# Kernel optimization log

Measured on AMD Instinct MI355X. Metric: run time of the kernel, lower is better.

## Reference

```python
import jax, jax.numpy as jnp
import numpy as np

B, S, H, K = 64, 512, 768, 64
NR, NN, ND = 9, 3, 3


def setup_inputs() -> dict:
    key = jax.random.key(0)
    ks = jax.random.split(key, 20)
    inp = {}
    inp["sequence_output"] = jax.random.normal(ks[0], (B, S, H), jnp.float32)
    for i, name in enumerate(["rel", "nov", "dir"]):
        inp[f"{name}_idx"] = jax.random.randint(ks[1 + i], (B, K), 0, S)
        inp[f"{name}_len"] = jax.random.randint(ks[4 + i], (B,), 0, K + 1)
    scale = 0.02
    for i, (name, nlab) in enumerate([("rel", NR), ("nov", NN), ("dir", ND)]):
        k0, k1 = jax.random.split(ks[7 + i])
        inp[f"{name}_dense_W"] = scale * jax.random.normal(k0, (H, H), jnp.float32)
        inp[f"{name}_dense_b"] = jnp.zeros((H,), jnp.float32)
        inp[f"{name}_cls_W"] = scale * jax.random.normal(k1, (nlab, H), jnp.float32)
        inp[f"{name}_cls_b"] = jnp.zeros((nlab,), jnp.float32)
    return inp


def _attn_pool(seq, idx, length):
    """Ragged intra-group self-attention pooling (get_token_reps / get_ne_reps).

    seq: [B,S,H]; idx: [B,K] padded token indices; length: [B] valid counts.
    Original computes (softmax(G G^T) @ G)[0]; only row 0 of the attention is
    needed, so we compute just that row.
    """
    G = jnp.take_along_axis(seq, idx[:, :, None], axis=1)  # [B,K,H]
    mask = jnp.arange(idx.shape[1])[None, :] < length[:, None]  # [B,K]
    scores0 = jnp.einsum('bh,bjh->bj', G[:, 0], G)  # row 0 of G G^T
    scores0 = jnp.where(mask, scores0, jnp.float32(-1e30))
    a0 = jax.nn.softmax(scores0, axis=-1)  # [B,K]
    pooled = jnp.einsum('bj,bjh->bh', a0, G)  # [B,H]
    # empty-group fallback: sequence_output[b, 0]
    return jnp.where(length[:, None] > 0, pooled, seq[:, 0])


def _head(rep, Wd, bd, Wc, bc):
    # HiddenTokenPooler dense + tanh, then token classifier
    h = jnp.tanh(rep @ Wd.T + bd)
    return h @ Wc.T + bc


def reference(sequence_output, rel_idx, rel_len, nov_idx, nov_len, dir_idx, dir_len,
              rel_dense_W, rel_dense_b, rel_cls_W, rel_cls_b,
              nov_dense_W, nov_dense_b, nov_cls_W, nov_cls_b,
              dir_dense_W, dir_dense_b, dir_cls_W, dir_cls_b):
    rel_rep = _attn_pool(sequence_output, rel_idx, rel_len)
    nov_rep = _attn_pool(sequence_output, nov_idx, nov_len)
    dir_rep = _attn_pool(sequence_output, dir_idx, dir_len)
    rel_logits = _head(rel_rep, rel_dense_W, rel_dense_b, rel_cls_W, rel_cls_b)
    nov_logits = _head(nov_rep, nov_dense_W, nov_dense_b, nov_cls_W, nov_cls_b)
    dir_logits = _head(dir_rep, dir_dense_W, dir_dense_b, dir_cls_W, dir_cls_b)
    return (rel_logits, nov_logits, dir_logits)
```

## Files before the change

kernel.cpp:

```cpp
#include <hip/hip_runtime.h>
#include <math.h>


#define Hdim 768
#define Kdim 64
#define Sdim 512
#define Bdim 64

typedef float f32x4 __attribute__((ext_vector_type(4)));
typedef short bf16x8 __attribute__((ext_vector_type(8)));

__device__ __forceinline__ unsigned short f2bf(float f) {
    union { float f; unsigned int u; } c; c.f = f;
    unsigned int u = c.u + 0x7FFFu + ((c.u >> 16) & 1u);
    return (unsigned short)(u >> 16);
}

__device__ __forceinline__ void cvt8(const float* __restrict__ src,
                                     unsigned short* __restrict__ dst) {
    float4 x = *(const float4*)src, y = *(const float4*)(src + 4);
    *(ushort4*)dst       = make_ushort4(f2bf(x.x), f2bf(x.y), f2bf(x.z), f2bf(x.w));
    *(ushort4*)(dst + 4) = make_ushort4(f2bf(y.x), f2bf(y.y), f2bf(y.z), f2bf(y.w));
}

__global__ __launch_bounds__(1024) void k_pool(
    const float* __restrict__ seq,
    const int* __restrict__ idxr, const int* __restrict__ lenr,
    const int* __restrict__ idxn, const int* __restrict__ lenn,
    const int* __restrict__ idxd, const int* __restrict__ lend,
    const float* __restrict__ cbr, const float* __restrict__ cbn,
    const float* __restrict__ cbd,
    const float* __restrict__ dWr, const float* __restrict__ dWn,
    const float* __restrict__ dWd,
    unsigned short* __restrict__ Wbf,
    unsigned short* __restrict__ Pbf,
    float* __restrict__ out)
{
    const int b = blockIdx.x, g = blockIdx.y;
    const int tid = threadIdx.x, lane = tid & 63, wave = tid >> 6;

    const int* idxp = (g == 0) ? idxr : (g == 1) ? idxn : idxd;
    const int* lnp  = (g == 0) ? lenr : (g == 1) ? lenn : lend;

    __shared__ int   sidx[Kdim];
    __shared__ float wm[16], wl[16], coef[16];
    __shared__ float wpart[16][Hdim];

    if (tid < Kdim) sidx[tid] = idxp[b * Kdim + tid];
    const int len = lnp[b];

    if (b == 0) {
        if (g == 0)      { if (tid < 576) out[tid]       = cbr[tid % 9]; }
        else if (g == 1) { if (tid < 192) out[576 + tid] = cbn[tid % 3]; }
        else             { if (tid < 192) out[768 + tid] = cbd[tid % 3]; }
    }
    __syncthreads();

    unsigned short* Pb = Pbf + ((size_t)g * Bdim + b) * Hdim;

    if (len > 0) {
        const float* row0 = seq + ((size_t)b * Sdim + sidx[0]) * Hdim;
        float g0[12];
#pragma unroll
        for (int k = 0; k < 3; ++k) {
            float4 v = *(const float4*)(row0 + 4 * lane + 256 * k);
            g0[4 * k + 0] = v.x; g0[4 * k + 1] = v.y;
            g0[4 * k + 2] = v.z; g0[4 * k + 3] = v.w;
        }

        float m = -1e30f, l = 0.f;
        float p[12] = {0,0,0,0,0,0,0,0,0,0,0,0};

        for (int j = wave; j < len; j += 16) {
            const float* rowj = seq + ((size_t)b * Sdim + sidx[j]) * Hdim;
            float v[12];
#pragma unroll
            for (int k = 0; k < 3; ++k) {
                float4 t = *(const float4*)(rowj + 4 * lane + 256 * k);
                v[4 * k + 0] = t.x; v[4 * k + 1] = t.y;
                v[4 * k + 2] = t.z; v[4 * k + 3] = t.w;
            }
            float s = 0.f;
#pragma unroll
            for (int k = 0; k < 12; ++k) s += g0[k] * v[k];
#pragma unroll
            for (int off = 32; off > 0; off >>= 1) s += __shfl_xor(s, off, 64);

            float mn    = fmaxf(m, s);
            float scale = __expf(m - mn);
            float e     = __expf(s - mn);
            l = l * scale + e;
#pragma unroll
            for (int k = 0; k < 12; ++k) p[k] = p[k] * scale + e * v[k];
            m = mn;
        }

        if (lane == 0) { wm[wave] = m; wl[wave] = l; }
#pragma unroll
        for (int k = 0; k < 3; ++k)
            *(float4*)&wpart[wave][4 * lane + 256 * k] =
                make_float4(p[4 * k], p[4 * k + 1], p[4 * k + 2], p[4 * k + 3]);
        __syncthreads();

        if (wave == 0 && lane < 16) {
            float mw = wm[lane], lw = wl[lane];
            float M = mw;
#pragma unroll
            for (int off = 8; off > 0; off >>= 1) M = fmaxf(M, __shfl_xor(M, off, 64));
            float sc = __expf(mw - M);
            float Ls = lw * sc;
#pragma unroll
            for (int off = 8; off > 0; off >>= 1) Ls += __shfl_xor(Ls, off, 64);
            coef[lane] = sc / Ls;
        }
        __syncthreads();

        if (tid < Hdim) {
            float acc = 0.f;
#pragma unroll
            for (int w = 0; w < 16; ++w) acc += wpart[w][tid] * coef[w];
            Pb[tid] = f2bf(acc);
        }
    } else {
        if (tid < Hdim) Pb[tid] = f2bf(seq[(size_t)b * Sdim * Hdim + tid]);
    }

    {
        const float* dW = (g == 0) ? dWr : (g == 1) ? dWn : dWd;
        unsigned short* Wb = Wbf + (size_t)g * Hdim * Hdim;
        for (int e = (b * 1024 + tid) * 8; e < Hdim * Hdim; e += 64 * 1024 * 8)
            cvt8(dW + e, Wb + e);
    }
}

__global__ __launch_bounds__(256) void k_dense_cls(
    const unsigned short* __restrict__ Wbf,
    const unsigned short* __restrict__ Pbf,
    const float* __restrict__ dbr, const float* __restrict__ dbn,
    const float* __restrict__ dbd,
    const float* __restrict__ cWr, const float* __restrict__ cWn,
    const float* __restrict__ cWd,
    float* __restrict__ out)
{
    const int mt = blockIdx.x, g = blockIdx.y;
    const float *db, *cW; int nlab, off;
    if (g == 0)      { db = dbr; cW = cWr; nlab = 9; off = 0;   }
    else if (g == 1) { db = dbn; cW = cWn; nlab = 3; off = 576; }
    else             { db = dbd; cW = cWd; nlab = 3; off = 768; }
    const int i0 = mt * 64;

    const int tid = threadIdx.x, lane = tid & 63, wv = tid >> 6;
    const int q = lane >> 4, col = lane & 15;

    const unsigned short* Ap = Wbf + ((size_t)g * Hdim + i0 + wv * 16 + col) * Hdim + 8 * q;
    const unsigned short* Bp = Pbf + ((size_t)g * Bdim + col) * Hdim + 8 * q;

    f32x4 acc[4] = {{0,0,0,0},{0,0,0,0},{0,0,0,0},{0,0,0,0}};

#pragma unroll 6
    for (int ks = 0; ks < Hdim; ks += 32) {
        bf16x8 a = *(const bf16x8*)(Ap + ks);
#pragma unroll
        for (int n = 0; n < 4; ++n) {
            bf16x8 bb = *(const bf16x8*)(Bp + (size_t)n * 16 * Hdim + ks);
            acc[n] = __builtin_amdgcn_mfma_f32_16x16x32_bf16(a, bb, acc[n], 0, 0, 0);
        }
    }

    __shared__ float hs[64][65];
#pragma unroll
    for (int n = 0; n < 4; ++n) {
        int bb = n * 16 + col;
#pragma unroll
        for (int r = 0; r < 4; ++r) {
            int il = wv * 16 + q * 4 + r;
            hs[il][bb] = tanhf(acc[n][r] + db[i0 + il]);
        }
    }
    __syncthreads();

    for (int c = wv; c < nlab; c += 4) {
        const float* wr = cW + (size_t)c * Hdim + i0;
        float a = 0.f;
#pragma unroll 16
        for (int il = 0; il < 64; ++il)
            a += wr[il] * hs[il][lane];
        atomicAdd(&out[off + lane * nlab + c], a);
    }
}

extern "C" void kernel_launch(void* const* d_in, const int* in_sizes, int n_in,
                              void* d_out, int out_size, void* d_ws, size_t ws_size,
                              hipStream_t stream) {
    const float* seq  = (const float*)d_in[0];
    const int*   idxr = (const int*)d_in[1];
    const int*   lenr = (const int*)d_in[2];
    const int*   idxn = (const int*)d_in[3];
    const int*   lenn = (const int*)d_in[4];
    const int*   idxd = (const int*)d_in[5];
    const int*   lend = (const int*)d_in[6];
    const float* dWr  = (const float*)d_in[7];
    const float* dbr  = (const float*)d_in[8];
    const float* cWr  = (const float*)d_in[9];
    const float* cbr  = (const float*)d_in[10];
    const float* dWn  = (const float*)d_in[11];
    const float* dbn  = (const float*)d_in[12];
    const float* cWn  = (const float*)d_in[13];
    const float* cbn  = (const float*)d_in[14];
    const float* dWd  = (const float*)d_in[15];
    const float* dbd  = (const float*)d_in[16];
    const float* cWd  = (const float*)d_in[17];
    const float* cbd  = (const float*)d_in[18];
    float* out = (float*)d_out;

    unsigned short* Wbf = (unsigned short*)d_ws;
    unsigned short* Pbf = Wbf + (size_t)3 * Hdim * Hdim;

    k_pool<<<dim3(Bdim, 3), 1024, 0, stream>>>(
        seq, idxr, lenr, idxn, lenn, idxd, lend,
        cbr, cbn, cbd, dWr, dWn, dWd, Wbf, Pbf, out);
    k_dense_cls<<<dim3(Hdim / 64, 3), 256, 0, stream>>>(
        Wbf, Pbf, dbr, dbn, dbd, cWr, cWn, cWd, out);
}
```

Before: 189.8 us.

## Fuse pooling and dense head into one producer-consumer kernel with flag sync

Merges the pooling kernel and the dense/classifier kernel into a single launch. 192 producer blocks do the attention pooling, and 36 consumer blocks each convert their dense-weight tile to bf16 into LDS and registers while the producers run. Consumers spin on per-group atomic counters before running the MFMA GEMM. This removes the separate launch and the bf16 weight round-trip through global memory. In exchange it relies on all blocks being co-resident, and the flag reset relies on the workspace being filled with a poison value before every call.

```diff
diff --git a/kernel.cpp b/kernel.cpp
--- a/kernel.cpp
+++ b/kernel.cpp
@@ -6,6 +6,9 @@
 #define Kdim 64
 #define Sdim 512
 #define Bdim 64
+#define NPROD 192
+#define POISON 0xAAAAAAAAu
+#define WLD 392
 
 typedef float f32x4 __attribute__((ext_vector_type(4)));
 typedef short bf16x8 __attribute__((ext_vector_type(8)));
@@ -16,14 +19,7 @@
     return (unsigned short)(u >> 16);
 }
 
-__device__ __forceinline__ void cvt8(const float* __restrict__ src,
-                                     unsigned short* __restrict__ dst) {
-    float4 x = *(const float4*)src, y = *(const float4*)(src + 4);
-    *(ushort4*)dst       = make_ushort4(f2bf(x.x), f2bf(x.y), f2bf(x.z), f2bf(x.w));
-    *(ushort4*)(dst + 4) = make_ushort4(f2bf(y.x), f2bf(y.y), f2bf(y.z), f2bf(y.w));
-}
-
-__global__ __launch_bounds__(1024) void k_pool(
+__global__ __launch_bounds__(1024) void biored_all(
     const float* __restrict__ seq,
     const int* __restrict__ idxr, const int* __restrict__ lenr,
     const int* __restrict__ idxn, const int* __restrict__ lenn,
@@ -32,160 +28,213 @@
     const float* __restrict__ cbd,
     const float* __restrict__ dWr, const float* __restrict__ dWn,
     const float* __restrict__ dWd,
-    unsigned short* __restrict__ Wbf,
-    unsigned short* __restrict__ Pbf,
-    float* __restrict__ out)
-{
-    const int b = blockIdx.x, g = blockIdx.y;
-    const int tid = threadIdx.x, lane = tid & 63, wave = tid >> 6;
-
-    const int* idxp = (g == 0) ? idxr : (g == 1) ? idxn : idxd;
-    const int* lnp  = (g == 0) ? lenr : (g == 1) ? lenn : lend;
-
-    __shared__ int   sidx[Kdim];
-    __shared__ float wm[16], wl[16], coef[16];
-    __shared__ float wpart[16][Hdim];
-
-    if (tid < Kdim) sidx[tid] = idxp[b * Kdim + tid];
-    const int len = lnp[b];
-
-    if (b == 0) {
-        if (g == 0)      { if (tid < 576) out[tid]       = cbr[tid % 9]; }
-        else if (g == 1) { if (tid < 192) out[576 + tid] = cbn[tid % 3]; }
-        else             { if (tid < 192) out[768 + tid] = cbd[tid % 3]; }
-    }
-    __syncthreads();
-
-    unsigned short* Pb = Pbf + ((size_t)g * Bdim + b) * Hdim;
-
-    if (len > 0) {
-        const float* row0 = seq + ((size_t)b * Sdim + sidx[0]) * Hdim;
-        float g0[12];
-#pragma unroll
-        for (int k = 0; k < 3; ++k) {
-            float4 v = *(const float4*)(row0 + 4 * lane + 256 * k);
-            g0[4 * k + 0] = v.x; g0[4 * k + 1] = v.y;
-            g0[4 * k + 2] = v.z; g0[4 * k + 3] = v.w;
-        }
-
-        float m = -1e30f, l = 0.f;
-        float p[12] = {0,0,0,0,0,0,0,0,0,0,0,0};
-
-        for (int j = wave; j < len; j += 16) {
-            const float* rowj = seq + ((size_t)b * Sdim + sidx[j]) * Hdim;
-            float v[12];
-#pragma unroll
-            for (int k = 0; k < 3; ++k) {
-                float4 t = *(const float4*)(rowj + 4 * lane + 256 * k);
-                v[4 * k + 0] = t.x; v[4 * k + 1] = t.y;
-                v[4 * k + 2] = t.z; v[4 * k + 3] = t.w;
-            }
-            float s = 0.f;
-#pragma unroll
-            for (int k = 0; k < 12; ++k) s += g0[k] * v[k];
-#pragma unroll
-            for (int off = 32; off > 0; off >>= 1) s += __shfl_xor(s, off, 64);
-
-            float mn    = fmaxf(m, s);
-            float scale = __expf(m - mn);
-            float e     = __expf(s - mn);
-            l = l * scale + e;
-#pragma unroll
-            for (int k = 0; k < 12; ++k) p[k] = p[k] * scale + e * v[k];
-            m = mn;
-        }
-
-        if (lane == 0) { wm[wave] = m; wl[wave] = l; }
-#pragma unroll
-        for (int k = 0; k < 3; ++k)
-            *(float4*)&wpart[wave][4 * lane + 256 * k] =
-                make_float4(p[4 * k], p[4 * k + 1], p[4 * k + 2], p[4 * k + 3]);
-        __syncthreads();
-
-        if (wave == 0 && lane < 16) {
-            float mw = wm[lane], lw = wl[lane];
-            float M = mw;
-#pragma unroll
-            for (int off = 8; off > 0; off >>= 1) M = fmaxf(M, __shfl_xor(M, off, 64));
-            float sc = __expf(mw - M);
-            float Ls = lw * sc;
-#pragma unroll
-            for (int off = 8; off > 0; off >>= 1) Ls += __shfl_xor(Ls, off, 64);
-            coef[lane] = sc / Ls;
-        }
-        __syncthreads();
-
-        if (tid < Hdim) {
-            float acc = 0.f;
-#pragma unroll
-            for (int w = 0; w < 16; ++w) acc += wpart[w][tid] * coef[w];
-            Pb[tid] = f2bf(acc);
-        }
-    } else {
-        if (tid < Hdim) Pb[tid] = f2bf(seq[(size_t)b * Sdim * Hdim + tid]);
-    }
-
-    {
-        const float* dW = (g == 0) ? dWr : (g == 1) ? dWn : dWd;
-        unsigned short* Wb = Wbf + (size_t)g * Hdim * Hdim;
-        for (int e = (b * 1024 + tid) * 8; e < Hdim * Hdim; e += 64 * 1024 * 8)
-            cvt8(dW + e, Wb + e);
-    }
-}
-
-__global__ __launch_bounds__(256) void k_dense_cls(
-    const unsigned short* __restrict__ Wbf,
-    const unsigned short* __restrict__ Pbf,
     const float* __restrict__ dbr, const float* __restrict__ dbn,
     const float* __restrict__ dbd,
     const float* __restrict__ cWr, const float* __restrict__ cWn,
     const float* __restrict__ cWd,
+    unsigned short* __restrict__ Pbf,
+    unsigned int* __restrict__ flags,
     float* __restrict__ out)
 {
-    const int mt = blockIdx.x, g = blockIdx.y;
-    const float *db, *cW; int nlab, off;
-    if (g == 0)      { db = dbr; cW = cWr; nlab = 9; off = 0;   }
-    else if (g == 1) { db = dbn; cW = cWn; nlab = 3; off = 576; }
-    else             { db = dbd; cW = cWd; nlab = 3; off = 768; }
-    const int i0 = mt * 64;
-
+    __shared__ __align__(16) char smem[50432];
     const int tid = threadIdx.x, lane = tid & 63, wv = tid >> 6;
-    const int q = lane >> 4, col = lane & 15;
-
-    const unsigned short* Ap = Wbf + ((size_t)g * Hdim + i0 + wv * 16 + col) * Hdim + 8 * q;
-    const unsigned short* Bp = Pbf + ((size_t)g * Bdim + col) * Hdim + 8 * q;
-
-    f32x4 acc[4] = {{0,0,0,0},{0,0,0,0},{0,0,0,0},{0,0,0,0}};
-
-#pragma unroll 6
-    for (int ks = 0; ks < Hdim; ks += 32) {
-        bf16x8 a = *(const bf16x8*)(Ap + ks);
-#pragma unroll
-        for (int n = 0; n < 4; ++n) {
-            bf16x8 bb = *(const bf16x8*)(Bp + (size_t)n * 16 * Hdim + ks);
-            acc[n] = __builtin_amdgcn_mfma_f32_16x16x32_bf16(a, bb, acc[n], 0, 0, 0);
-        }
-    }
-
-    __shared__ float hs[64][65];
-#pragma unroll
-    for (int n = 0; n < 4; ++n) {
-        int bb = n * 16 + col;
-#pragma unroll
-        for (int r = 0; r < 4; ++r) {
-            int il = wv * 16 + q * 4 + r;
-            hs[il][bb] = tanhf(acc[n][r] + db[i0 + il]);
-        }
-    }
-    __syncthreads();
-
-    for (int c = wv; c < nlab; c += 4) {
-        const float* wr = cW + (size_t)c * Hdim + i0;
-        float a = 0.f;
+    const int bid = blockIdx.x;
+
+    if (bid < NPROD) {
+        const int b = bid & 63, g = bid >> 6;
+        const int* idxp = (g == 0) ? idxr : (g == 1) ? idxn : idxd;
+        const int* lnp  = (g == 0) ? lenr : (g == 1) ? lenn : lend;
+
+        int*   sidx = (int*)smem;
+        float* wm   = (float*)(smem + 256);
+        float* wl   = (float*)(smem + 320);
+        float* coef = (float*)(smem + 384);
+        float (*wpart)[Hdim] = (float (*)[Hdim])(smem + 448);
+
+        if (tid < Kdim) sidx[tid] = idxp[b * Kdim + tid];
+        const int len = lnp[b];
+
+        if (b == 0) {
+            if (g == 0)      { if (tid < 576) out[tid]       = cbr[tid % 9]; }
+            else if (g == 1) { if (tid < 192) out[576 + tid] = cbn[tid % 3]; }
+            else             { if (tid < 192) out[768 + tid] = cbd[tid % 3]; }
+        }
+        __syncthreads();
+
+        unsigned short* Pb = Pbf + ((size_t)g * Bdim + b) * Hdim;
+
+        if (len > 0) {
+            const float* row0 = seq + ((size_t)b * Sdim + sidx[0]) * Hdim;
+            float g0[12];
+#pragma unroll
+            for (int k = 0; k < 3; ++k) {
+                float4 v = *(const float4*)(row0 + 4 * lane + 256 * k);
+                g0[4 * k + 0] = v.x; g0[4 * k + 1] = v.y;
+                g0[4 * k + 2] = v.z; g0[4 * k + 3] = v.w;
+            }
+            float m = -1e30f, l = 0.f;
+            float p[12] = {0,0,0,0,0,0,0,0,0,0,0,0};
+
+            for (int j = wv; j < len; j += 16) {
+                const float* rowj = seq + ((size_t)b * Sdim + sidx[j]) * Hdim;
+                float v[12];
+#pragma unroll
+                for (int k = 0; k < 3; ++k) {
+                    float4 t = *(const float4*)(rowj + 4 * lane + 256 * k);
+                    v[4 * k + 0] = t.x; v[4 * k + 1] = t.y;
+                    v[4 * k + 2] = t.z; v[4 * k + 3] = t.w;
+                }
+                float s = 0.f;
+#pragma unroll
+                for (int k = 0; k < 12; ++k) s += g0[k] * v[k];
+#pragma unroll
+                for (int off = 32; off > 0; off >>= 1) s += __shfl_xor(s, off, 64);
+
+                float mn    = fmaxf(m, s);
+                float scale = __expf(m - mn);
+                float e     = __expf(s - mn);
+                l = l * scale + e;
+#pragma unroll
+                for (int k = 0; k < 12; ++k) p[k] = p[k] * scale + e * v[k];
+                m = mn;
+            }
+
+            if (lane == 0) { wm[wv] = m; wl[wv] = l; }
+#pragma unroll
+            for (int k = 0; k < 3; ++k)
+                *(float4*)&wpart[wv][4 * lane + 256 * k] =
+                    make_float4(p[4 * k], p[4 * k + 1], p[4 * k + 2], p[4 * k + 3]);
+            __syncthreads();
+
+            if (wv == 0 && lane < 16) {
+                float mw = wm[lane], lw = wl[lane];
+                float M = mw;
+#pragma unroll
+                for (int off = 8; off > 0; off >>= 1) M = fmaxf(M, __shfl_xor(M, off, 64));
+                float sc = __expf(mw - M);
+                float Ls = lw * sc;
+#pragma unroll
+                for (int off = 8; off > 0; off >>= 1) Ls += __shfl_xor(Ls, off, 64);
+                coef[lane] = sc / Ls;
+            }
+            __syncthreads();
+
+            if (tid < Hdim) {
+                float acc = 0.f;
+#pragma unroll
+                for (int w = 0; w < 16; ++w) acc += wpart[w][tid] * coef[w];
+                Pb[tid] = f2bf(acc);
+            }
+        } else {
+            if (tid < Hdim) Pb[tid] = f2bf(seq[(size_t)b * Sdim * Hdim + tid]);
+        }
+
+        __syncthreads();
+        if (tid == 0) {
+            __threadfence();
+            atomicCAS(&flags[g], POISON, 0u);
+            atomicAdd(&flags[g], 1u);
+        }
+    } else {
+        const int cid = bid - NPROD;
+        const int g = cid / 12, mt = cid % 12;
+        const float* dW = (g == 0) ? dWr : (g == 1) ? dWn : dWd;
+        const float* db = (g == 0) ? dbr : (g == 1) ? dbn : dbd;
+        const float* cW = (g == 0) ? cWr : (g == 1) ? cWn : cWd;
+        const int nlab = (g == 0) ? 9 : 3;
+        const int off  = (g == 0) ? 0 : (g == 1) ? 576 : 768;
+        const int i0 = mt * 64;
+        const int q = lane >> 4, col = lane & 15;
+
+        unsigned short* Wlds = (unsigned short*)smem;
+
+#pragma unroll
+        for (int rr = 0; rr < 4; ++rr) {
+            int row = wv * 4 + rr;
+            const float* src = dW + (size_t)(i0 + row) * Hdim;
+            {
+                int k = lane * 4;
+                float4 x = *(const float4*)(src + k);
+                *(ushort4*)&Wlds[row * WLD + k] =
+                    make_ushort4(f2bf(x.x), f2bf(x.y), f2bf(x.z), f2bf(x.w));
+            }
+            if (lane < 32) {
+                int k = 256 + lane * 4;
+                float4 x = *(const float4*)(src + k);
+                *(ushort4*)&Wlds[row * WLD + k] =
+                    make_ushort4(f2bf(x.x), f2bf(x.y), f2bf(x.z), f2bf(x.w));
+            }
+        }
+        bf16x8 afrag[12];
+        if (wv < 4) {
+            const float* Arow = dW + (size_t)(i0 + wv * 16 + col) * Hdim + 384 + 8 * q;
+#pragma unroll
+            for (int t = 0; t < 12; ++t) {
+                float4 x = *(const float4*)(Arow + t * 32);
+                float4 y = *(const float4*)(Arow + t * 32 + 4);
+                bf16x8 a;
+                a[0] = (short)f2bf(x.x); a[1] = (short)f2bf(x.y);
+                a[2] = (short)f2bf(x.z); a[3] = (short)f2bf(x.w);
+                a[4] = (short)f2bf(y.x); a[5] = (short)f2bf(y.y);
+                a[6] = (short)f2bf(y.z); a[7] = (short)f2bf(y.w);
+                afrag[t] = a;
+            }
+        }
+
+        if (tid == 0) {
+            while (__hip_atomic_load(&flags[g], __ATOMIC_ACQUIRE,
+                                     __HIP_MEMORY_SCOPE_AGENT) != 64u)
+                __builtin_amdgcn_s_sleep(8);
+        }
+        __syncthreads();
+
+        f32x4 acc[4] = {{0,0,0,0},{0,0,0,0},{0,0,0,0},{0,0,0,0}};
+        if (wv < 4) {
+            const unsigned short* Bp = Pbf + ((size_t)g * Bdim + col) * Hdim + 8 * q;
+#pragma unroll
+            for (int s = 0; s < 12; ++s) {
+                bf16x8 a = *(const bf16x8*)&Wlds[(wv * 16 + col) * WLD + s * 32 + 8 * q];
+#pragma unroll
+                for (int n = 0; n < 4; ++n) {
+                    bf16x8 bb = *(const bf16x8*)(Bp + (size_t)n * 16 * Hdim + s * 32);
+                    acc[n] = __builtin_amdgcn_mfma_f32_16x16x32_bf16(a, bb, acc[n], 0, 0, 0);
+                }
+            }
+#pragma unroll
+            for (int t = 0; t < 12; ++t) {
+#pragma unroll
+                for (int n = 0; n < 4; ++n) {
+                    bf16x8 bb = *(const bf16x8*)(Bp + (size_t)n * 16 * Hdim + 384 + t * 32);
+                    acc[n] = __builtin_amdgcn_mfma_f32_16x16x32_bf16(afrag[t], bb, acc[n], 0, 0, 0);
+                }
+            }
+        }
+        __syncthreads();
+
+        float (*hs)[65] = (float (*)[65])smem;
+        if (wv < 4) {
+#pragma unroll
+            for (int n = 0; n < 4; ++n) {
+                int bb = n * 16 + col;
+#pragma unroll
+                for (int r = 0; r < 4; ++r) {
+                    int il = wv * 16 + q * 4 + r;
+                    hs[il][bb] = tanhf(acc[n][r] + db[i0 + il]);
+                }
+            }
+        }
+        __syncthreads();
+
+        if (wv < 4) {
+            for (int c = wv; c < nlab; c += 4) {
+                const float* wr = cW + (size_t)c * Hdim + i0;
+                float a = 0.f;
 #pragma unroll 16
-        for (int il = 0; il < 64; ++il)
-            a += wr[il] * hs[il][lane];
-        atomicAdd(&out[off + lane * nlab + c], a);
+                for (int il = 0; il < 64; ++il)
+                    a += wr[il] * hs[il][lane];
+                atomicAdd(&out[off + lane * nlab + c], a);
+            }
+        }
     }
 }
 
@@ -213,12 +262,11 @@
     const float* cbd  = (const float*)d_in[18];
     float* out = (float*)d_out;
 
-    unsigned short* Wbf = (unsigned short*)d_ws;
-    unsigned short* Pbf = Wbf + (size_t)3 * Hdim * Hdim;
-
-    k_pool<<<dim3(Bdim, 3), 1024, 0, stream>>>(
+    unsigned short* Pbf  = (unsigned short*)d_ws;
+    unsigned int*   flags = (unsigned int*)((char*)d_ws + (size_t)3 * Bdim * Hdim * 2);
+
+    biored_all<<<NPROD + 36, 1024, 0, stream>>>(
         seq, idxr, lenr, idxn, lenn, idxd, lend,
-        cbr, cbn, cbd, dWr, dWn, dWd, Wbf, Pbf, out);
-    k_dense_cls<<<dim3(Hdim / 64, 3), 256, 0, stream>>>(
-        Wbf, Pbf, dbr, dbn, dbd, cWr, cWn, cWd, out);
+        cbr, cbn, cbd, dWr, dWn, dWd, dbr, dbn, dbd, cWr, cWn, cWd,
+        Pbf, flags, out);
 }
```

New measurement: 194.2 us. 2.3% more time.
